# Kernel optimization log

Measured on AMD Instinct MI355X. Metric: run time of the kernel, lower is better.

## Reference

```python
import jax, jax.numpy as jnp
import numpy as np

B, C, H, W = 16, 512, 32, 32

def _conv2d(x, w, b, pad):
    y = jax.lax.conv_general_dilated(
        x, w, window_strides=(1, 1), padding=[(pad, pad), (pad, pad)],
        dimension_numbers=('NCHW', 'OIHW', 'NCHW'))
    return y + b[None, :, None, None]

def setup_inputs() -> dict:
    key = jax.random.key(0)
    ks = jax.random.split(key, 10)
    s3 = 1.0 / np.sqrt(C * 9)   # torch conv2d default init scale (3x3)
    s1 = 1.0 / np.sqrt(3 * C)   # 1x1 conv over 3C input channels
    return {
        'x':  jax.random.normal(ks[0], (B, C, H, W), jnp.float32),
        'w1': jax.random.uniform(ks[1], (C, C, 3, 3), jnp.float32, -s3, s3),
        'b1': jax.random.uniform(ks[2], (C,), jnp.float32, -s3, s3),
        'w2': jax.random.uniform(ks[3], (C, C, 3, 3), jnp.float32, -s3, s3),
        'b2': jax.random.uniform(ks[4], (C,), jnp.float32, -s3, s3),
        'w3': jax.random.uniform(ks[5], (C, C, 3, 3), jnp.float32, -s3, s3),
        'b3': jax.random.uniform(ks[6], (C,), jnp.float32, -s3, s3),
        'alpha': jax.random.normal(ks[7], (), jnp.float32) * 0.1,
        'beta':  jax.random.normal(ks[8], (), jnp.float32) * 0.1,
        'wf': jax.random.uniform(ks[9], (C, 3 * C, 1, 1), jnp.float32, -s1, s1),
        'bf': jnp.zeros((C,), jnp.float32),
    }

def reference(x, w1, b1, w2, b2, w3, b3, alpha, beta, wf, bf):
    b, c, h, w = x.shape
    n = h * w
    # --- spatial attention ---
    A = _conv2d(x, w1, b1, 1).reshape(b, c, n)  # [b,C,N]
    Bm = _conv2d(x, w2, b2, 1).reshape(b, c, n)
    D = _conv2d(x, w3, b3, 1).reshape(b, c, n)
    M = jnp.einsum('bcn,bcm->bnm', A, Bm)       # A^T @ B, [b,N,N]
    M = jax.nn.softmax(M, axis=-1)
    # weighted_C = M @ D^T -> [b,N,C]; then permute to [b,C,N]
    spat = jnp.einsum('bnm,bcm->bcn', M, D).reshape(b, c, h, w)
    spat = alpha * spat
    # --- channel attention ---
    Xr = x.reshape(b, c, n)                     # [b,C,N]
    S = jnp.einsum('bcn,bdn->bcd', Xr, Xr)      # [b,C,C]
    S = jax.nn.softmax(S, axis=-1)
    # weighted = S^T @ Xr
    chan = jnp.einsum('bdc,bdn->bcn', S, Xr).reshape(b, c, h, w)
    chan = beta * chan
    # --- fuse ---
    cat = jnp.concatenate((x, spat, chan), axis=1)  # [b,3C,H,W]
    return _conv2d(cat, wf, bf, 0)
```

## Files before the change

### kernel.cpp

```cpp
#include <hip/hip_runtime.h>
#include <hip/hip_bf16.h>
#include <stdint.h>

#define B_   16
#define C_   512
#define N_   1024
#define C3   1536
#define NPAD 1156

using bf16x8 = __attribute__((ext_vector_type(8))) __bf16;
using f32x4  = __attribute__((ext_vector_type(4))) float;
typedef unsigned short ushort_t;

__device__ __forceinline__ ushort_t f2bf(float f) {
    union { float f; uint32_t u; } v; v.f = f;
    uint32_t r = v.u + 0x7FFFu + ((v.u >> 16) & 1u);
    return (ushort_t)(r >> 16);
}

typedef __attribute__((address_space(3))) void lds_void_t;
typedef const __attribute__((address_space(1))) void g_void_t;
__device__ __forceinline__ void gload16(const void* g, void* l) {
    __builtin_amdgcn_global_load_lds((g_void_t*)g, (lds_void_t*)l, 16, 0, 0);
}


__global__ void castwf_kernel(const float* __restrict__ wf,
                              ushort_t* __restrict__ Wfb,
                              ushort_t* __restrict__ zp,
                              const float* __restrict__ b1,
                              const float* __restrict__ b2,
                              const float* __restrict__ b3,
                              float* __restrict__ b_all) {
    int idx = blockIdx.x * 256 + threadIdx.x;
    if (idx < 512) zp[idx] = 0;
    if (idx < 1536) b_all[idx] = (idx < 512) ? b1[idx] : (idx < 1024) ? b2[idx - 512] : b3[idx - 1024];
    Wfb[idx] = f2bf(wf[idx]);
}

__global__ void castw_kernel(const float* __restrict__ w,
                             ushort_t* __restrict__ Wall, int coff) {
    int idx = blockIdx.x * 256 + threadIdx.x;
    int t = idx / (C_ * C_);
    int rem = idx - t * (C_ * C_);
    Wall[(size_t)t * (C3 * C_) + (size_t)coff * C_ + rem] = f2bf(w[(size_t)rem * 9 + t]);
}

__global__ void castx_kernel(const float* __restrict__ x,
                             ushort_t* __restrict__ Xb,
                             ushort_t* __restrict__ cat,
                             ushort_t* __restrict__ catP) {
    __shared__ ushort_t t[32][33];
    int n0 = blockIdx.x * 32, c0 = blockIdx.y * 32, b = blockIdx.z;
    int tx = threadIdx.x & 31, ty = threadIdx.x >> 5;
    const float* xb = x + ((size_t)b * C_ + c0) * N_ + n0;
#pragma unroll
    for (int q = 0; q < 4; ++q) {
        int c = ty + q * 8;
        ushort_t h = f2bf(xb[(size_t)c * N_ + tx]);
        Xb[((size_t)b * C_ + c0 + c) * N_ + n0 + tx] = h;
        t[c][tx] = h;
    }
    __syncthreads();
#pragma unroll
    for (int q = 0; q < 4; ++q) {
        int n = ty + q * 8;
        ushort_t v = t[tx][n];
        cat[((size_t)b * N_ + n0 + n) * C3 + c0 + tx] = v;
        int prow = (n0 >> 5) * 34 + n + 35;
        catP[((size_t)b * NPAD + prow) * C_ + c0 + tx] = v;
    }
}

__global__ void transp_kernel(const ushort_t* __restrict__ Y,
                              ushort_t* __restrict__ Db) {
    __shared__ ushort_t t[32][33];
    int n0 = blockIdx.x * 32, c0 = blockIdx.y * 32, b = blockIdx.z;
    int tx = threadIdx.x & 31, ty = threadIdx.x >> 5;
#pragma unroll
    for (int q = 0; q < 4; ++q) {
        int n = ty + q * 8;
        t[n][tx] = Y[((size_t)b * N_ + n0 + n) * C3 + 1024 + c0 + tx];
    }
    __syncthreads();
#pragma unroll
    for (int q = 0; q < 4; ++q) {
        int c = ty + q * 8;
        Db[((size_t)b * C_ + c0 + c) * N_ + n0 + tx] = t[tx][c];
    }
}

__global__ void softmax_kernel(float* __restrict__ Mb) {
    int n = blockIdx.x, b = blockIdx.y;
    float* row = Mb + ((size_t)b * N_ + n) * N_;
    int tid = threadIdx.x;
    float4 v = ((const float4*)row)[tid];
    float m = fmaxf(fmaxf(v.x, v.y), fmaxf(v.z, v.w));
#pragma unroll
    for (int off = 1; off < 64; off <<= 1) m = fmaxf(m, __shfl_xor(m, off));
    __shared__ float sm[4], ss[4];
    int wid = tid >> 6, lane = tid & 63;
    if (lane == 0) sm[wid] = m;
    __syncthreads();
    m = fmaxf(fmaxf(sm[0], sm[1]), fmaxf(sm[2], sm[3]));
    float e0 = __expf(v.x - m), e1 = __expf(v.y - m);
    float e2 = __expf(v.z - m), e3 = __expf(v.w - m);
    float s = e0 + e1 + e2 + e3;
#pragma unroll
    for (int off = 1; off < 64; off <<= 1) s += __shfl_xor(s, off);
    if (lane == 0) ss[wid] = s;
    __syncthreads();
    s = ss[0] + ss[1] + ss[2] + ss[3];
    float r = 1.0f / s;
    ushort4 o;
    o.x = f2bf(e0 * r); o.y = f2bf(e1 * r); o.z = f2bf(e2 * r); o.w = f2bf(e3 * r);
    ((ushort4*)row)[tid] = o;
}

__global__ void rowstats_kernel(const float* __restrict__ S,
                                float* __restrict__ mxv, float* __restrict__ rzv) {
    int c = blockIdx.x, b = blockIdx.y;
    const float* row = S + ((size_t)b * C_ + c) * C_;
    int tid = threadIdx.x;
    float2 v = ((const float2*)row)[tid];
    float m = fmaxf(v.x, v.y);
#pragma unroll
    for (int off = 1; off < 64; off <<= 1) m = fmaxf(m, __shfl_xor(m, off));
    __shared__ float sm[4], ss[4];
    int wid = tid >> 6, lane = tid & 63;
    if (lane == 0) sm[wid] = m;
    __syncthreads();
    m = fmaxf(fmaxf(sm[0], sm[1]), fmaxf(sm[2], sm[3]));
    float e = __expf(v.x - m) + __expf(v.y - m);
#pragma unroll
    for (int off = 1; off < 64; off <<= 1) e += __shfl_xor(e, off);
    if (lane == 0) ss[wid] = e;
    __syncthreads();
    if (tid == 0) {
        e = ss[0] + ss[1] + ss[2] + ss[3];
        mxv[(size_t)b * C_ + c] = m;
        rzv[(size_t)b * C_ + c] = 1.0f / e;
    }
}

__global__ void sst_kernel(const float* __restrict__ S,
                           const float* __restrict__ mxv, const float* __restrict__ rzv,
                           ushort_t* __restrict__ Sst) {
    int idx = blockIdx.x * 256 + threadIdx.x;
    int d = idx & (C_ - 1);
    int b = idx >> 18;
    float st = mxv[((size_t)b << 9) + d];
    float rz = rzv[((size_t)b << 9) + d];
    Sst[idx] = f2bf(__expf(S[idx] - st) * rz);
}

#define BM 128
#define BN 128
#define BKk 64

template <int XMODE, int OUTF32, int BIASMODE, int SCALE, int SWZ>
__global__ __launch_bounds__(256)
void gemm_bt_kernel(const ushort_t* __restrict__ Ab, int lda, long long strideA, long long tapA,
                    const ushort_t* __restrict__ Bb, int ldb, long long strideB, long long tapB,
                    void* __restrict__ Cb, int ldc, long long strideC,
                    int K, int ntaps,
                    const float* __restrict__ bias,
                    const float* __restrict__ scaleptr,
                    const ushort_t* __restrict__ zpage) {
    __shared__ short As[BM * BKk];
    __shared__ short Bs[BN * BKk];
    int tid = threadIdx.x;
    int wid = tid >> 6, lane = tid & 63;
    int wr = wid >> 1, wc = wid & 1;
    int j0 = blockIdx.x * BN, i0 = blockIdx.y * BM, b = blockIdx.z;
    const ushort_t* Abase = Ab + (size_t)b * strideA;
    const ushort_t* Bbase = Bb + (size_t)b * strideB;

    f32x4 acc[4][4] = {};

    int rs = wid * 32 + (lane >> 3);
    int kb = (lane & 7) * 8;

    for (int tap = 0; tap < ntaps; ++tap) {
        const ushort_t* At_ = Abase + (size_t)tap * tapA;
        const ushort_t* Bt_ = Bbase + (size_t)tap * tapB;
        const ushort_t* aq[4];
        const ushort_t* bq[4];
#pragma unroll
        for (int q = 0; q < 4; ++q)
            aq[q] = At_ + (size_t)(i0 + rs + q * 8) * lda + kb;
#pragma unroll
        for (int q = 0; q < 4; ++q)
            bq[q] = Bt_ + (size_t)(j0 + rs + q * 8) * ldb + kb;

        for (int kk = 0; kk < K; kk += BKk) {
            __syncthreads();
#pragma unroll
            for (int q = 0; q < 4; ++q) {
                gload16(aq[q], &As[(wid * 32 + q * 8) * BKk]);
                aq[q] += BKk;
                gload16(bq[q], &Bs[(wid * 32 + q * 8) * BKk]);
                bq[q] += BKk;
            }
            __syncthreads();
#pragma unroll
            for (int kc = 0; kc < BKk; kc += 32) {
                bf16x8 af[4], bfr[4];
#pragma unroll
                for (int m = 0; m < 4; ++m)
                    af[m] = *(const bf16x8*)&As[(wr * 64 + m * 16 + (lane & 15)) * BKk + kc + (lane >> 4) * 8];
#pragma unroll
                for (int nb = 0; nb < 4; ++nb)
                    bfr[nb] = *(const bf16x8*)&Bs[(wc * 64 + nb * 16 + (lane & 15)) * BKk + kc + (lane >> 4) * 8];
#pragma unroll
                for (int m = 0; m < 4; ++m)
#pragma unroll
                    for (int nb = 0; nb < 4; ++nb)
                        acc[m][nb] = __builtin_amdgcn_mfma_f32_16x16x32_bf16(af[m], bfr[nb], acc[m][nb], 0, 0, 0);
            }
        }
    }

    float scale = SCALE ? *scaleptr : 1.0f;
#pragma unroll
    for (int m = 0; m < 4; ++m) {
#pragma unroll
        for (int nb = 0; nb < 4; ++nb) {
            int i = i0 + wr * 64 + m * 16 + (lane >> 4) * 4;
            int j = j0 + wc * 64 + nb * 16 + (lane & 15);
#pragma unroll
            for (int r = 0; r < 4; ++r) {
                float v = acc[m][nb][r];
                if (BIASMODE == 1) v += bias[i + r];
                if (BIASMODE == 2) v += bias[j];
                if (SCALE) v *= scale;
                if (OUTF32)
                    ((float*)Cb)[(size_t)b * strideC + (size_t)(i + r) * ldc + j] = v;
                else
                    ((ushort_t*)Cb)[(size_t)b * strideC + (size_t)(i + r) * ldc + j] = f2bf(v);
            }
        }
    }
}

#define R3BM 256
#define R3BN 128
#define R3BK 64

template <int XMODE, int OUTF32, int BIASMODE, int SCALE>
__global__ __launch_bounds__(512, 2)
void gemm_r3_kernel(const ushort_t* __restrict__ Ab, int lda, long long strideA, long long tapA,
                    const ushort_t* __restrict__ Bb, int ldb, long long strideB, long long tapB,
                    void* __restrict__ Cb, int ldc, long long strideC,
                    int K, int ntaps,
                    const float* __restrict__ bias,
                    const float* __restrict__ scaleptr,
                    const ushort_t* __restrict__ zpage) {
    __shared__ short As[3][R3BM * R3BK];
    __shared__ short Bs[3][R3BN * R3BK];
    int tid = threadIdx.x;
    int wid = tid >> 6, lane = tid & 63;
    int wr = wid >> 1, wc = wid & 1;
    int j0 = blockIdx.x * R3BN, i0 = blockIdx.y * R3BM, b = blockIdx.z;
    int kpt = K >> 6;
    int nt = ntaps * kpt;

    f32x4 acc[4][4] = {};

    int sr = tid >> 3;
    int klds = (tid & 7) * 8;
    int sbase = wid * 512;

    int aoff[4][2], boff[4][2];
#pragma unroll
    for (int m = 0; m < 4; ++m) {
        int row = wr * 64 + m * 16 + (lane & 15);
        int sw = (row & 7) << 3;
#pragma unroll
        for (int h = 0; h < 2; ++h)
            aoff[m][h] = row * R3BK + ((h * 32 + (lane >> 4) * 8) ^ sw);
    }
#pragma unroll
    for (int nb = 0; nb < 4; ++nb) {
        int row = wc * 64 + nb * 16 + (lane & 15);
        int sw = (row & 7) << 3;
#pragma unroll
        for (int h = 0; h < 2; ++h)
            boff[nb][h] = row * R3BK + ((h * 32 + (lane >> 4) * 8) ^ sw);
    }

    const ushort_t* pa[4];
    const ushort_t* pb[2];
#pragma unroll
    for (int s = 0; s < 4; ++s) {
        int r = sr + s * 64;
        int ks = klds ^ ((r & 7) << 3);
        if (XMODE == 1) {
            int li = (i0 & (N_ - 1)) + r;
            int pr = (li >> 5) * 34 + (li & 31) + 35;
            pa[s] = Ab + ((size_t)(i0 >> 10) * NPAD + pr) * lda + ks;
        } else {
            pa[s] = Ab + (size_t)b * strideA + (size_t)(i0 + r) * lda + ks;
        }
    }
#pragma unroll
    for (int s = 0; s < 2; ++s) {
        int r = sr + s * 64;
        int ks = klds ^ ((r & 7) << 3);
        pb[s] = Bb + (size_t)b * strideB + (size_t)(j0 + r) * ldb + ks;
    }

    int s_tap = 0, s_kk = 0;
    auto STAGE = [&](int slot) {
        long long uA, uB;
        if (XMODE == 1) {
            int dh = s_tap / 3 - 1, dw = s_tap - (s_tap / 3) * 3 - 1;
            uA = (long long)(dh * 34 + dw) * lda + s_kk * R3BK;
        } else {
            uA = (long long)s_tap * tapA + (long long)s_kk * R3BK;
        }
        uB = (long long)s_tap * tapB + (long long)s_kk * R3BK;
#pragma unroll
        for (int s = 0; s < 4; ++s)
            gload16(pa[s] + uA, &As[slot][sbase + s * 4096]);
#pragma unroll
        for (int s = 0; s < 2; ++s)
            gload16(pb[s] + uB, &Bs[slot][sbase + s * 4096]);
        if (++s_tap == ntaps) { s_tap = 0; ++s_kk; }
    };

    STAGE(0);
    STAGE(1);

    for (int t = 0; t < nt; ++t) {
        int slot = t - (t / 3) * 3;
        if (t + 1 < nt) asm volatile("s_waitcnt vmcnt(6)" ::: "memory");
        else            asm volatile("s_waitcnt vmcnt(0)" ::: "memory");
        __builtin_amdgcn_s_barrier();
        __builtin_amdgcn_sched_barrier(0);

        const short* Aslot = &As[slot][0];
        const short* Bslot = &Bs[slot][0];
        bf16x8 af[4][2], bfr[4][2];
#pragma unroll
        for (int h = 0; h < 2; ++h) {
#pragma unroll
            for (int m = 0; m < 4; ++m)
                af[m][h] = *(const bf16x8*)&Aslot[aoff[m][h]];
#pragma unroll
            for (int nb = 0; nb < 4; ++nb)
                bfr[nb][h] = *(const bf16x8*)&Bslot[boff[nb][h]];
        }

        if (t + 2 < nt) STAGE((t + 2) - ((t + 2) / 3) * 3);

        asm volatile("s_waitcnt lgkmcnt(8)" ::: "memory");
        __builtin_amdgcn_sched_barrier(0);
        __builtin_amdgcn_s_setprio(1);
#pragma unroll
        for (int m = 0; m < 4; ++m)
#pragma unroll
            for (int nb = 0; nb < 4; ++nb)
                acc[m][nb] = __builtin_amdgcn_mfma_f32_16x16x32_bf16(af[m][0], bfr[nb][0], acc[m][nb], 0, 0, 0);
        asm volatile("s_waitcnt lgkmcnt(0)" ::: "memory");
        __builtin_amdgcn_sched_barrier(0);
#pragma unroll
        for (int m = 0; m < 4; ++m)
#pragma unroll
            for (int nb = 0; nb < 4; ++nb)
                acc[m][nb] = __builtin_amdgcn_mfma_f32_16x16x32_bf16(af[m][1], bfr[nb][1], acc[m][nb], 0, 0, 0);
        __builtin_amdgcn_s_setprio(0);
    }

    float scale = SCALE ? *scaleptr : 1.0f;
#pragma unroll
    for (int m = 0; m < 4; ++m) {
#pragma unroll
        for (int nb = 0; nb < 4; ++nb) {
            int i = i0 + wr * 64 + m * 16 + (lane >> 4) * 4;
            int j = j0 + wc * 64 + nb * 16 + (lane & 15);
#pragma unroll
            for (int r = 0; r < 4; ++r) {
                float v = acc[m][nb][r];
                if (BIASMODE == 1) v += bias[i + r];
                if (BIASMODE == 2) v += bias[j];
                if (SCALE) v *= scale;
                if (OUTF32)
                    ((float*)Cb)[(size_t)b * strideC + (size_t)(i + r) * ldc + j] = v;
                else
                    ((ushort_t*)Cb)[(size_t)b * strideC + (size_t)(i + r) * ldc + j] = f2bf(v);
            }
        }
    }
}

constexpr size_t OFF_ZP   = 0;
constexpr size_t OFF_BALL = 1024;
constexpr size_t OFF_WFB  = OFF_BALL + 6144;
constexpr size_t OFF_CAT  = OFF_WFB + (size_t)C_ * C3 * 2;
constexpr size_t OFF_Y    = OFF_CAT + (size_t)B_ * N_ * C3 * 2;
constexpr size_t OFF_DB   = OFF_Y + (size_t)B_ * N_ * C3 * 2;
constexpr size_t OFF_SR   = OFF_DB + (size_t)B_ * C_ * N_ * 2;
constexpr size_t OFF_SST  = OFF_SR + (size_t)B_ * C_ * C_ * 4;
constexpr size_t OFF_MX   = OFF_SST + (size_t)B_ * C_ * C_ * 2;
constexpr size_t OFF_RZ   = OFF_MX + (size_t)B_ * C_ * 4;
constexpr size_t OFF_U    = OFF_RZ + (size_t)B_ * C_ * 4;
constexpr size_t WALL_SZ  = (size_t)9 * C3 * C_ * 2;
constexpr size_t XB_SZ    = (size_t)B_ * C_ * N_ * 2;
constexpr size_t CATP_SZ  = (size_t)B_ * NPAD * C_ * 2;
constexpr size_t OFF_WALL = OFF_U;
constexpr size_t OFF_XB   = OFF_U + WALL_SZ;
constexpr size_t OFF_CATP = OFF_XB + XB_SZ;
constexpr size_t OFF_M    = OFF_U;
constexpr size_t EXT_A    = OFF_CATP + CATP_SZ;
constexpr size_t EXT_B    = OFF_M + (size_t)B_ * N_ * N_ * 4;
constexpr size_t WS_NEED  = EXT_A > EXT_B ? EXT_A : EXT_B;

extern "C" void kernel_launch(void* const* d_in, const int* in_sizes, int n_in,
                              void* d_out, int out_size, void* d_ws, size_t ws_size,
                              hipStream_t stream) {
    const float* x   = (const float*)d_in[0];
    const float* w1  = (const float*)d_in[1];
    const float* b1  = (const float*)d_in[2];
    const float* w2  = (const float*)d_in[3];
    const float* b2  = (const float*)d_in[4];
    const float* w3  = (const float*)d_in[5];
    const float* b3  = (const float*)d_in[6];
    const float* alpha = (const float*)d_in[7];
    const float* beta  = (const float*)d_in[8];
    const float* wf  = (const float*)d_in[9];
    const float* bfv = (const float*)d_in[10];
    float* out = (float*)d_out;
    char* ws = (char*)d_ws;
    if (ws_size < WS_NEED) return;

    ushort_t* zp   = (ushort_t*)(ws + OFF_ZP);
    float*    ball = (float*)(ws + OFF_BALL);
    ushort_t* Wfb  = (ushort_t*)(ws + OFF_WFB);
    ushort_t* cat  = (ushort_t*)(ws + OFF_CAT);
    ushort_t* Y    = (ushort_t*)(ws + OFF_Y);
    ushort_t* Db   = (ushort_t*)(ws + OFF_DB);
    float*    Sr   = (float*)(ws + OFF_SR);
    ushort_t* Sst  = (ushort_t*)(ws + OFF_SST);
    float*    mxv  = (float*)(ws + OFF_MX);
    float*    rzv  = (float*)(ws + OFF_RZ);
    ushort_t* Wall = (ushort_t*)(ws + OFF_WALL);
    ushort_t* Xb   = (ushort_t*)(ws + OFF_XB);
    ushort_t* catP = (ushort_t*)(ws + OFF_CATP);
    float*    Mb   = (float*)(ws + OFF_M);

    hipMemsetAsync(catP, 0, CATP_SZ, stream);

    castwf_kernel<<<(C_ * C3) / 256, 256, 0, stream>>>(wf, Wfb, zp, b1, b2, b3, ball);
    castw_kernel<<<(9 * C_ * C_) / 256, 256, 0, stream>>>(w1, Wall, 0);
    castw_kernel<<<(9 * C_ * C_) / 256, 256, 0, stream>>>(w2, Wall, 512);
    castw_kernel<<<(9 * C_ * C_) / 256, 256, 0, stream>>>(w3, Wall, 1024);
    castx_kernel<<<dim3(N_ / 32, C_ / 32, B_), 256, 0, stream>>>(x, Xb, cat, catP);

    for (int c = 0; c < 3; ++c) {
        gemm_r3_kernel<1, 0, 2, 0><<<dim3(4, 64, 1), 512, 0, stream>>>(
            catP, C_, 0, 0,
            Wall + (size_t)c * 512 * C_, C_, 0, (long long)C3 * C_,
            Y + (size_t)c * 512, C3, 0,
            C_, 9, ball + c * 512, nullptr, zp);
    }
    transp_kernel<<<dim3(N_ / 32, C_ / 32, B_), 256, 0, stream>>>(Y, Db);
    gemm_bt_kernel<0, 1, 0, 0, 0><<<dim3(4, 4, B_), 256, 0, stream>>>(
        Xb, N_, (long long)C_ * N_, 0,
        Xb, N_, (long long)C_ * N_, 0,
        Sr, C_, (long long)C_ * C_,
        N_, 1, nullptr, nullptr, zp);
    rowstats_kernel<<<dim3(C_, B_), 256, 0, stream>>>(Sr, mxv, rzv);
    sst_kernel<<<(B_ * C_ * C_) / 256, 256, 0, stream>>>(Sr, mxv, rzv, Sst);
    gemm_r3_kernel<0, 1, 0, 0><<<dim3(8, 4, B_), 512, 0, stream>>>(
        Y, C3, (long long)N_ * C3, 0,
        Y + 512, C3, (long long)N_ * C3, 0,
        Mb, N_, (long long)N_ * N_,
        C_, 1, nullptr, nullptr, zp);
    softmax_kernel<<<dim3(N_, B_), 256, 0, stream>>>(Mb);
    gemm_r3_kernel<0, 0, 0, 1><<<dim3(4, 4, B_), 512, 0, stream>>>(
        (const ushort_t*)Mb, 2048, (long long)N_ * 2048, 0,
        Db, N_, (long long)C_ * N_, 0,
        cat + 512, C3, (long long)N_ * C3,
        N_, 1, nullptr, alpha, zp);
    gemm_r3_kernel<0, 0, 0, 1><<<dim3(4, 4, B_), 512, 0, stream>>>(
        cat, C3, (long long)N_ * C3, 0,
        Sst, C_, (long long)C_ * C_, 0,
        cat + 1024, C3, (long long)N_ * C3,
        C_, 1, nullptr, beta, zp);
    gemm_r3_kernel<0, 1, 1, 0><<<dim3(8, 2, B_), 512, 0, stream>>>(
        Wfb, C3, 0, 0,
        cat, C3, (long long)N_ * C3, 0,
        out, N_, (long long)C_ * N_,
        C3, 1, bfv, nullptr, zp);
}
```

Baseline: 445.9 us.

## Replace 256x128x64 GEMM tile with 128x128x32 tile kernel

Replaces the 512-thread GEMM kernel (256x128 tile, K-step 64) with a 256-thread kernel using 128x128 tiles and K-step 32, and adjusts the LDS swizzle, load mapping, wait counts and every launch grid to match. The smaller tile doubles the number of blocks, and the smaller LDS footprint allows three blocks per CU. This is meant to give better occupancy and wave count across the CUs. In exchange it halves the work per barrier, doubling the loop iterations, and lowers operand reuse per global load.

```diff
diff --git a/kernel.cpp b/kernel.cpp
--- a/kernel.cpp
+++ b/kernel.cpp
@@ -243,58 +243,52 @@
     }
 }
 
-#define R3BM 256
-#define R3BN 128
-#define R3BK 64
+#define P2BM 128
+#define P2BN 128
+#define P2BK 32
 
 template <int XMODE, int OUTF32, int BIASMODE, int SCALE>
-__global__ __launch_bounds__(512, 2)
-void gemm_r3_kernel(const ushort_t* __restrict__ Ab, int lda, long long strideA, long long tapA,
+__global__ __launch_bounds__(256, 3)
+void gemm_p2_kernel(const ushort_t* __restrict__ Ab, int lda, long long strideA, long long tapA,
                     const ushort_t* __restrict__ Bb, int ldb, long long strideB, long long tapB,
                     void* __restrict__ Cb, int ldc, long long strideC,
                     int K, int ntaps,
                     const float* __restrict__ bias,
-                    const float* __restrict__ scaleptr,
-                    const ushort_t* __restrict__ zpage) {
-    __shared__ short As[3][R3BM * R3BK];
-    __shared__ short Bs[3][R3BN * R3BK];
+                    const float* __restrict__ scaleptr) {
+    __shared__ short As[3][P2BM * P2BK];
+    __shared__ short Bs[3][P2BN * P2BK];
     int tid = threadIdx.x;
     int wid = tid >> 6, lane = tid & 63;
     int wr = wid >> 1, wc = wid & 1;
-    int j0 = blockIdx.x * R3BN, i0 = blockIdx.y * R3BM, b = blockIdx.z;
-    int kpt = K >> 6;
+    int j0 = blockIdx.x * P2BN, i0 = blockIdx.y * P2BM, b = blockIdx.z;
+    int kpt = K >> 5;
     int nt = ntaps * kpt;
 
     f32x4 acc[4][4] = {};
 
-    int sr = tid >> 3;
-    int klds = (tid & 7) * 8;
-    int sbase = wid * 512;
-
-    int aoff[4][2], boff[4][2];
-#pragma unroll
-    for (int m = 0; m < 4; ++m) {
-        int row = wr * 64 + m * 16 + (lane & 15);
-        int sw = (row & 7) << 3;
-#pragma unroll
-        for (int h = 0; h < 2; ++h)
-            aoff[m][h] = row * R3BK + ((h * 32 + (lane >> 4) * 8) ^ sw);
-    }
-#pragma unroll
-    for (int nb = 0; nb < 4; ++nb) {
-        int row = wc * 64 + nb * 16 + (lane & 15);
-        int sw = (row & 7) << 3;
-#pragma unroll
-        for (int h = 0; h < 2; ++h)
-            boff[nb][h] = row * R3BK + ((h * 32 + (lane >> 4) * 8) ^ sw);
-    }
-
-    const ushort_t* pa[4];
+    int sr = tid >> 2;
+    int klds = (tid & 3) * 8;
+    int ssw = ((sr >> 1) & 3) << 3;
+    int sdst = tid * 8;
+
+    int aoff[4], boff[4];
+    {
+        int fk = (lane >> 4) * 8;
+        int rsw = (((lane & 15) >> 1) & 3) << 3;
+#pragma unroll
+        for (int m = 0; m < 4; ++m)
+            aoff[m] = (wr * 64 + m * 16 + (lane & 15)) * P2BK + (fk ^ rsw);
+#pragma unroll
+        for (int nb = 0; nb < 4; ++nb)
+            boff[nb] = (wc * 64 + nb * 16 + (lane & 15)) * P2BK + (fk ^ rsw);
+    }
+
+    const ushort_t* pa[2];
     const ushort_t* pb[2];
 #pragma unroll
-    for (int s = 0; s < 4; ++s) {
+    for (int s = 0; s < 2; ++s) {
         int r = sr + s * 64;
-        int ks = klds ^ ((r & 7) << 3);
+        int ks = klds ^ ssw;
         if (XMODE == 1) {
             int li = (i0 & (N_ - 1)) + r;
             int pr = (li >> 5) * 34 + (li & 31) + 35;
@@ -302,11 +296,6 @@
         } else {
             pa[s] = Ab + (size_t)b * strideA + (size_t)(i0 + r) * lda + ks;
         }
-    }
-#pragma unroll
-    for (int s = 0; s < 2; ++s) {
-        int r = sr + s * 64;
-        int ks = klds ^ ((r & 7) << 3);
         pb[s] = Bb + (size_t)b * strideB + (size_t)(j0 + r) * ldb + ks;
     }
 
@@ -315,17 +304,17 @@
         long long uA, uB;
         if (XMODE == 1) {
             int dh = s_tap / 3 - 1, dw = s_tap - (s_tap / 3) * 3 - 1;
-            uA = (long long)(dh * 34 + dw) * lda + s_kk * R3BK;
+            uA = (long long)(dh * 34 + dw) * lda + s_kk * P2BK;
         } else {
-            uA = (long long)s_tap * tapA + (long long)s_kk * R3BK;
+            uA = (long long)s_tap * tapA + (long long)s_kk * P2BK;
         }
-        uB = (long long)s_tap * tapB + (long long)s_kk * R3BK;
-#pragma unroll
-        for (int s = 0; s < 4; ++s)
-            gload16(pa[s] + uA, &As[slot][sbase + s * 4096]);
+        uB = (long long)s_tap * tapB + (long long)s_kk * P2BK;
 #pragma unroll
         for (int s = 0; s < 2; ++s)
-            gload16(pb[s] + uB, &Bs[slot][sbase + s * 4096]);
+            gload16(pa[s] + uA, &As[slot][sdst + s * 2048]);
+#pragma unroll
+        for (int s = 0; s < 2; ++s)
+            gload16(pb[s] + uB, &Bs[slot][sdst + s * 2048]);
         if (++s_tap == ntaps) { s_tap = 0; ++s_kk; }
     };
 
@@ -334,41 +323,31 @@
 
     for (int t = 0; t < nt; ++t) {
         int slot = t - (t / 3) * 3;
-        if (t + 1 < nt) asm volatile("s_waitcnt vmcnt(6)" ::: "memory");
+        if (t + 1 < nt) asm volatile("s_waitcnt vmcnt(4)" ::: "memory");
         else            asm volatile("s_waitcnt vmcnt(0)" ::: "memory");
         __builtin_amdgcn_s_barrier();
         __builtin_amdgcn_sched_barrier(0);
 
         const short* Aslot = &As[slot][0];
         const short* Bslot = &Bs[slot][0];
-        bf16x8 af[4][2], bfr[4][2];
-#pragma unroll
-        for (int h = 0; h < 2; ++h) {
-#pragma unroll
-            for (int m = 0; m < 4; ++m)
-                af[m][h] = *(const bf16x8*)&Aslot[aoff[m][h]];
-#pragma unroll
-            for (int nb = 0; nb < 4; ++nb)
-                bfr[nb][h] = *(const bf16x8*)&Bslot[boff[nb][h]];
-        }
+        bf16x8 af[4], bfr[4];
+#pragma unroll
+        for (int m = 0; m < 4; ++m)
+            af[m] = *(const bf16x8*)&Aslot[aoff[m]];
+#pragma unroll
+        for (int nb = 0; nb < 4; ++nb)
+            bfr[nb] = *(const bf16x8*)&Bslot[boff[nb]];
 
         if (t + 2 < nt) STAGE((t + 2) - ((t + 2) / 3) * 3);
 
-        asm volatile("s_waitcnt lgkmcnt(8)" ::: "memory");
+        asm volatile("s_waitcnt lgkmcnt(0)" ::: "memory");
         __builtin_amdgcn_sched_barrier(0);
         __builtin_amdgcn_s_setprio(1);
 #pragma unroll
         for (int m = 0; m < 4; ++m)
 #pragma unroll
             for (int nb = 0; nb < 4; ++nb)
-                acc[m][nb] = __builtin_amdgcn_mfma_f32_16x16x32_bf16(af[m][0], bfr[nb][0], acc[m][nb], 0, 0, 0);
-        asm volatile("s_waitcnt lgkmcnt(0)" ::: "memory");
-        __builtin_amdgcn_sched_barrier(0);
-#pragma unroll
-        for (int m = 0; m < 4; ++m)
-#pragma unroll
-            for (int nb = 0; nb < 4; ++nb)
-                acc[m][nb] = __builtin_amdgcn_mfma_f32_16x16x32_bf16(af[m][1], bfr[nb][1], acc[m][nb], 0, 0, 0);
+                acc[m][nb] = __builtin_amdgcn_mfma_f32_16x16x32_bf16(af[m], bfr[nb], acc[m][nb], 0, 0, 0);
         __builtin_amdgcn_s_setprio(0);
     }
 
@@ -458,11 +437,11 @@
     castx_kernel<<<dim3(N_ / 32, C_ / 32, B_), 256, 0, stream>>>(x, Xb, cat, catP);
 
     for (int c = 0; c < 3; ++c) {
-        gemm_r3_kernel<1, 0, 2, 0><<<dim3(4, 64, 1), 512, 0, stream>>>(
+        gemm_p2_kernel<1, 0, 2, 0><<<dim3(4, 128, 1), 256, 0, stream>>>(
             catP, C_, 0, 0,
             Wall + (size_t)c * 512 * C_, C_, 0, (long long)C3 * C_,
             Y + (size_t)c * 512, C3, 0,
-            C_, 9, ball + c * 512, nullptr, zp);
+            C_, 9, ball + c * 512, nullptr);
     }
     transp_kernel<<<dim3(N_ / 32, C_ / 32, B_), 256, 0, stream>>>(Y, Db);
     gemm_bt_kernel<0, 1, 0, 0, 0><<<dim3(4, 4, B_), 256, 0, stream>>>(
@@ -472,25 +451,25 @@
         N_, 1, nullptr, nullptr, zp);
     rowstats_kernel<<<dim3(C_, B_), 256, 0, stream>>>(Sr, mxv, rzv);
     sst_kernel<<<(B_ * C_ * C_) / 256, 256, 0, stream>>>(Sr, mxv, rzv, Sst);
-    gemm_r3_kernel<0, 1, 0, 0><<<dim3(8, 4, B_), 512, 0, stream>>>(
+    gemm_p2_kernel<0, 1, 0, 0><<<dim3(8, 8, B_), 256, 0, stream>>>(
         Y, C3, (long long)N_ * C3, 0,
         Y + 512, C3, (long long)N_ * C3, 0,
         Mb, N_, (long long)N_ * N_,
-        C_, 1, nullptr, nullptr, zp);
+        C_, 1, nullptr, nullptr);
     softmax_kernel<<<dim3(N_, B_), 256, 0, stream>>>(Mb);
-    gemm_r3_kernel<0, 0, 0, 1><<<dim3(4, 4, B_), 512, 0, stream>>>(
+    gemm_p2_kernel<0, 0, 0, 1><<<dim3(4, 8, B_), 256, 0, stream>>>(
         (const ushort_t*)Mb, 2048, (long long)N_ * 2048, 0,
         Db, N_, (long long)C_ * N_, 0,
         cat + 512, C3, (long long)N_ * C3,
-        N_, 1, nullptr, alpha, zp);
-    gemm_r3_kernel<0, 0, 0, 1><<<dim3(4, 4, B_), 512, 0, stream>>>(
+        N_, 1, nullptr, alpha);
+    gemm_p2_kernel<0, 0, 0, 1><<<dim3(4, 8, B_), 256, 0, stream>>>(
         cat, C3, (long long)N_ * C3, 0,
         Sst, C_, (long long)C_ * C_, 0,
         cat + 1024, C3, (long long)N_ * C3,
-        C_, 1, nullptr, beta, zp);
-    gemm_r3_kernel<0, 1, 1, 0><<<dim3(8, 2, B_), 512, 0, stream>>>(
+        C_, 1, nullptr, beta);
+    gemm_p2_kernel<0, 1, 1, 0><<<dim3(8, 4, B_), 256, 0, stream>>>(
         Wfb, C3, 0, 0,
         cat, C3, (long long)N_ * C3, 0,
         out, N_, (long long)C_ * N_,
-        C3, 1, bfv, nullptr, zp);
-}
+        C3, 1, bfv, nullptr);
+}
```

Measured after the change: 497.7 us. 11.6% more time.
